# Optimization experiments

Measured on AMD Instinct MI355X. Metric: run time of the kernel, lower is better.

## Reference

```python
import jax, jax.numpy as jnp
import numpy as np

RCR = 5.2
RCA = 3.5
ETA_R = 16.0
SHF_R = jnp.asarray(np.linspace(0.9, 4.93125, 16), dtype=jnp.float32)  # 16 radial shifts
SHF_Z = jnp.asarray(np.array([0.19634954, 0.58904862, 0.9817477, 1.3744468,
                              1.7671459, 2.1598449, 2.552544, 2.9452431]), dtype=jnp.float32)
ETA_A = 8.0
ZETA = 32.0
SHF_A = jnp.asarray(np.array([0.9, 1.55, 2.2, 2.85]), dtype=jnp.float32)
NUM_SPECIES = 4  # consts file defines 4 species; module forces all atoms to species 0


def _cutoff(d, rc):
    return jnp.where(d <= rc, 0.5 * jnp.cos(jnp.pi * d / rc) + 0.5, 0.0)


def _aev(coords):
    n = coords.shape[0]
    diff = coords[:, None, :] - coords[None, :, :]             # [i,j,3]
    eye = jnp.eye(n, dtype=bool)
    d2 = jnp.sum(diff * diff, axis=-1)
    d = jnp.sqrt(jnp.where(eye, 1.0, d2))                      # safe sqrt on the diagonal
    # ---- radial subAEV: 0.25 * exp(-EtaR*(d-ShfR)^2) * fc(d, Rcr), summed over neighbors j
    fc_r = jnp.where(eye, 0.0, _cutoff(d, RCR))
    rad = 0.25 * jnp.exp(-ETA_R * (d[:, :, None] - SHF_R) ** 2) * fc_r[:, :, None]
    radial = jnp.sum(rad, axis=1)                              # (n, 16)
    # ---- angular subAEV
    fc_a = jnp.where(eye, 0.0, _cutoff(d, RCA))
    unit = diff / d[:, :, None]
    cos_t = jnp.einsum('ijc,ikc->ijk', unit, unit)             # cos angle(j-i-k)
    theta = jnp.arccos(0.95 * cos_t)                           # torchani's 0.95 stabilizer
    f1 = ((1.0 + jnp.cos(theta[..., None] - SHF_Z)) * 0.5) ** ZETA            # (n,n,n,8)
    davg = 0.5 * (d[:, :, None] + d[:, None, :])               # (d_ij + d_ik)/2
    # zero out j==i, k==i (via fc_a) and j==k; ordered (j,k) sum == torchani's 2*sum over j<k
    pairmask = (fc_a[:, :, None] * fc_a[:, None, :]) * (~eye)[None, :, :]
    f2 = jnp.exp(-ETA_A * (davg[..., None] - SHF_A) ** 2) * pairmask[..., None]  # (n,n,n,4)
    ang = jnp.einsum('ijka,ijkz->iaz', f2, f1).reshape(n, -1)  # (n, 32), (ShfA, ShfZ) order
    # ---- embed into 4-species AEV layout (only species-0 blocks are nonzero)
    radial_full = jnp.concatenate(
        [radial, jnp.zeros((n, 16 * (NUM_SPECIES - 1)), radial.dtype)], axis=1)   # (n, 64)
    n_pairs = NUM_SPECIES * (NUM_SPECIES + 1) // 2
    angular_full = jnp.concatenate(
        [ang, jnp.zeros((n, 32 * (n_pairs - 1)), ang.dtype)], axis=1)             # (n, 320)
    return jnp.concatenate([radial_full, angular_full], axis=1)                    # (n, 384)


def setup_inputs() -> dict:
    key = jax.random.key(0)
    # ~200-atom cluster, coordinates in Angstrom-scale cloud so cutoffs are populated
    coordinates = jax.random.normal(key, (200, 3), dtype=jnp.float32) * 4.0
    return {"coordinates": coordinates}


def reference(coordinates):
    return _aev(coordinates)
```

## Files before the change

kernel.cpp:

```cpp
#include <hip/hip_runtime.h>
#include <math.h>

#define RCR 5.2f
#define RCA 3.5f
#define ETA_R 16.0f
#define ETA_A 8.0f
#define PI_F 3.14159265358979323846f
#define MAXN 256

template <int CTRL, int ROW_MASK>
__device__ __forceinline__ float dpp_add(float v) {
    int s = __builtin_amdgcn_update_dpp(0, __float_as_int(v), CTRL, ROW_MASK, 0xf, true);
    return v + __int_as_float(s);
}
__device__ __forceinline__ float wave64_sum(float v) {
    v = dpp_add<0x111, 0xf>(v);
    v = dpp_add<0x112, 0xf>(v);
    v = dpp_add<0x114, 0xf>(v);
    v = dpp_add<0x118, 0xf>(v);
    v = dpp_add<0x142, 0xa>(v);
    v = dpp_add<0x143, 0xc>(v);
    return v;
}

__global__ __launch_bounds__(256) void aev_kernel(const float* __restrict__ coords,
                                                  float* __restrict__ out, int n) {
    const int i = blockIdx.x;
    const int tid = threadIdx.x;
    const int lane = tid & 63;
    const int wv = tid >> 6;

    __shared__ float sx[MAXN], sy[MAXN], sz[MAXN];
    __shared__ float4 njd[MAXN];
    __shared__ float nfc[MAXN];
    __shared__ int s_wcnt[4];
    __shared__ float s_rad[16];
    __shared__ float s_ang[32];

    if (tid < n) {
        sx[tid] = coords[3 * tid + 0];
        sy[tid] = coords[3 * tid + 1];
        sz[tid] = coords[3 * tid + 2];
    }
    if (tid < 16) s_rad[tid] = 0.0f;
    if (tid < 32) s_ang[tid] = 0.0f;
    __syncthreads();

    const float xi = sx[i], yi = sy[i], zi = sz[i];

    const int j = tid;
    const bool valid = (j < n) && (j != i);
    float dx = 0.f, dy = 0.f, dz = 0.f, d = 1.0e9f;
    if (valid) {
        dx = xi - sx[j]; dy = yi - sy[j]; dz = zi - sz[j];
        d = sqrtf(dx * dx + dy * dy + dz * dz);
    }
    const float fcr = (d <= RCR) ? (0.5f * __cosf(d * (PI_F / RCR)) + 0.5f) : 0.0f;
    float racc[16];
#pragma unroll
    for (int r = 0; r < 16; r++) {
        const float t = d - (0.9f + 0.26875f * (float)r);
        racc[r] = fcr * __expf(-ETA_R * t * t);
    }

    const bool pred = valid && (d <= RCA);
    const unsigned long long bmask = __ballot(pred);
    if (lane == 0) s_wcnt[wv] = __popcll(bmask);
    __syncthreads();
    int base = 0;
#pragma unroll
    for (int w = 0; w < 4; w++) if (w < wv) base += s_wcnt[w];
    const int m = s_wcnt[0] + s_wcnt[1] + s_wcnt[2] + s_wcnt[3];
    if (pred) {
        const int slot = base + __popcll(bmask & ((1ULL << lane) - 1ULL));
        const float inv = 1.0f / d;
        njd[slot] = make_float4(dx * inv, dy * inv, dz * inv, d);
        nfc[slot] = 0.5f * __cosf(d * (PI_F / RCA)) + 0.5f;
    }

#pragma unroll
    for (int r = 0; r < 16; r++) {
        const float v = wave64_sum(racc[r]);
        if (lane == 63) atomicAdd(&s_rad[r], v);
    }
    __syncthreads();

    const float cZ[8] = { 0.98078528f,  0.83146961f,  0.55557023f,  0.19509032f,
                         -0.19509032f, -0.55557023f, -0.83146961f, -0.98078528f};
    const float sZ[8] = { 0.19509032f,  0.55557023f,  0.83146961f,  0.98078528f,
                          0.98078528f,  0.83146961f,  0.55557023f,  0.19509032f};
    float aacc[32];
#pragma unroll
    for (int c = 0; c < 32; c++) aacc[c] = 0.0f;

    const int T = m * (m - 1) / 2;
    for (int p = tid; p < T; p += 256) {
        int jj = (int)((1.0f + sqrtf(8.0f * (float)p + 1.0f)) * 0.5f);
        while (jj * (jj - 1) / 2 > p) jj--;
        while ((jj + 1) * jj / 2 <= p) jj++;
        const int kk = p - jj * (jj - 1) / 2;

        const float4 a = njd[jj];
        const float4 b = njd[kk];
        const float ct = 0.95f * (a.x * b.x + a.y * b.y + a.z * b.z);
        const float st = sqrtf(fmaxf(0.0f, 1.0f - ct * ct));
        const float davg = 0.5f * (a.w + b.w);
        const float fcp = nfc[jj] * nfc[kk];

        float f2[4];
#pragma unroll
        for (int aa = 0; aa < 4; aa++) {
            const float t = davg - (0.9f + 0.65f * (float)aa);
            f2[aa] = fcp * __expf(-ETA_A * t * t);
        }
#pragma unroll
        for (int z = 0; z < 8; z++) {
            const float x = fmaf(ct, cZ[z], fmaf(st, sZ[z], 1.0f)) * 0.5f;
            float t2 = x * x; t2 *= t2; t2 *= t2; t2 *= t2; t2 *= t2;
#pragma unroll
            for (int aa = 0; aa < 4; aa++)
                aacc[aa * 8 + z] = fmaf(f2[aa], t2, aacc[aa * 8 + z]);
        }
    }

#pragma unroll
    for (int c = 0; c < 32; c++) {
        const float v = wave64_sum(aacc[c]);
        if (lane == 63) atomicAdd(&s_ang[c], v);
    }
    __syncthreads();

    float* row = out + (size_t)i * 384;
    for (int c = tid; c < 384; c += 256) {
        float v = 0.0f;
        if (c < 16) v = 0.25f * s_rad[c];
        else if (c >= 64 && c < 96) v = 2.0f * s_ang[c - 64];
        row[c] = v;
    }
}

extern "C" void kernel_launch(void* const* d_in, const int* in_sizes, int n_in,
                              void* d_out, int out_size, void* d_ws, size_t ws_size,
                              hipStream_t stream) {
    const float* coords = (const float*)d_in[0];
    float* out = (float*)d_out;
    const int n = in_sizes[0] / 3;
    aev_kernel<<<n, 256, 0, stream>>>(coords, out, n);
}
```

Before: 58.44 us.

## Vectorize coord load, replace LDS atomics with per-wave slots, recurrence for angular exps

Coordinates are now loaded into a single interleaved shared array with float4 copies, and the output row is written as float4. The shared-memory atomicAdds used for the radial and angular reductions are replaced by per-wave slots that are summed at write-out time. The four angular Gaussian exponentials are computed from two __expf calls and a multiplicative recurrence over the equally spaced shifts, cutting transcendental work in the hot pair loop. The recurrence can lose some precision or underflow differently than direct evaluation, and the float4 casts assume 16-byte aligned input and output pointers.

```diff
diff --git a/kernel.cpp b/kernel.cpp
--- a/kernel.cpp
+++ b/kernel.cpp
@@ -30,29 +30,33 @@
     const int lane = tid & 63;
     const int wv = tid >> 6;
 
-    __shared__ float sx[MAXN], sy[MAXN], sz[MAXN];
+    __shared__ __align__(16) float scoord[3 * MAXN];
     __shared__ float4 njd[MAXN];
     __shared__ float nfc[MAXN];
     __shared__ int s_wcnt[4];
-    __shared__ float s_rad[16];
-    __shared__ float s_ang[32];
+    __shared__ float s_radw[4][16];
+    __shared__ float s_angw[4][32];
 
-    if (tid < n) {
-        sx[tid] = coords[3 * tid + 0];
-        sy[tid] = coords[3 * tid + 1];
-        sz[tid] = coords[3 * tid + 2];
+    {
+        const int total = 3 * n;
+        const int n4 = total >> 2;
+        if (tid < n4) {
+            ((float4*)scoord)[tid] = ((const float4*)coords)[tid];
+        } else if (tid == n4) {
+            for (int c = n4 * 4; c < total; c++) scoord[c] = coords[c];
+        }
     }
-    if (tid < 16) s_rad[tid] = 0.0f;
-    if (tid < 32) s_ang[tid] = 0.0f;
     __syncthreads();
 
-    const float xi = sx[i], yi = sy[i], zi = sz[i];
+    const float xi = scoord[3 * i + 0], yi = scoord[3 * i + 1], zi = scoord[3 * i + 2];
 
     const int j = tid;
     const bool valid = (j < n) && (j != i);
     float dx = 0.f, dy = 0.f, dz = 0.f, d = 1.0e9f;
     if (valid) {
-        dx = xi - sx[j]; dy = yi - sy[j]; dz = zi - sz[j];
+        dx = xi - scoord[3 * j + 0];
+        dy = yi - scoord[3 * j + 1];
+        dz = zi - scoord[3 * j + 2];
         d = sqrtf(dx * dx + dy * dy + dz * dz);
     }
     const float fcr = (d <= RCR) ? (0.5f * __cosf(d * (PI_F / RCR)) + 0.5f) : 0.0f;
@@ -81,7 +85,7 @@
 #pragma unroll
     for (int r = 0; r < 16; r++) {
         const float v = wave64_sum(racc[r]);
-        if (lane == 63) atomicAdd(&s_rad[r], v);
+        if (lane == 63) s_radw[wv][r] = v;
     }
     __syncthreads();
 
@@ -107,12 +111,16 @@
         const float davg = 0.5f * (a.w + b.w);
         const float fcp = nfc[jj] * nfc[kk];
 
+        const float dv0 = davg - 0.9f;
+        float t0 = __expf(-ETA_A * dv0 * dv0);
+        float u = __expf(fmaf(10.4f, davg, -12.74f));
+        const float w = 0.00115743f;
         float f2[4];
-#pragma unroll
-        for (int aa = 0; aa < 4; aa++) {
-            const float t = davg - (0.9f + 0.65f * (float)aa);
-            f2[aa] = fcp * __expf(-ETA_A * t * t);
-        }
+        f2[0] = fcp * t0;
+        t0 *= u; u *= w; f2[1] = fcp * t0;
+        t0 *= u; u *= w; f2[2] = fcp * t0;
+        t0 *= u;         f2[3] = fcp * t0;
+
 #pragma unroll
         for (int z = 0; z < 8; z++) {
             const float x = fmaf(ct, cZ[z], fmaf(st, sZ[z], 1.0f)) * 0.5f;
@@ -126,16 +134,29 @@
 #pragma unroll
     for (int c = 0; c < 32; c++) {
         const float v = wave64_sum(aacc[c]);
-        if (lane == 63) atomicAdd(&s_ang[c], v);
+        if (lane == 63) s_angw[wv][c] = v;
     }
     __syncthreads();
 
-    float* row = out + (size_t)i * 384;
-    for (int c = tid; c < 384; c += 256) {
-        float v = 0.0f;
-        if (c < 16) v = 0.25f * s_rad[c];
-        else if (c >= 64 && c < 96) v = 2.0f * s_ang[c - 64];
-        row[c] = v;
+    float4* row4 = (float4*)(out + (size_t)i * 384);
+    for (int c4 = tid; c4 < 96; c4 += 256) {
+        float4 v = make_float4(0.f, 0.f, 0.f, 0.f);
+        if (c4 < 4) {
+            const int c = 4 * c4;
+            float* p = &v.x;
+#pragma unroll
+            for (int q = 0; q < 4; q++)
+                p[q] = 0.25f * (s_radw[0][c + q] + s_radw[1][c + q] +
+                                s_radw[2][c + q] + s_radw[3][c + q]);
+        } else if (c4 >= 16 && c4 < 24) {
+            const int c = 4 * (c4 - 16);
+            float* p = &v.x;
+#pragma unroll
+            for (int q = 0; q < 4; q++)
+                p[q] = 2.0f * (s_angw[0][c + q] + s_angw[1][c + q] +
+                               s_angw[2][c + q] + s_angw[3][c + q]);
+        }
+        row4[c4] = v;
     }
 }
 
```

Result: faster. 56.02 us (-4.1%).
